# Kernel optimization log

Hardware: AMD Instinct MI355X
Metric: run time of the kernel (lower is better)

Reference implementation:

```python
import jax, jax.numpy as jnp
import numpy as np

N_NODES = 50000
N_EDGES = 800000
F_IN = 256
F_OUT = 64
HEADS = 4
LEAKY_ALPHA = 0.2


def setup_inputs() -> dict:
    key = jax.random.key(0)
    ks = jax.random.split(key, 8)
    x = jax.random.normal(ks[0], (N_NODES, F_IN), dtype=jnp.float32)
    W = jax.random.normal(ks[1], (HEADS, F_IN, F_OUT), dtype=jnp.float32) * 0.05
    a_self = jax.random.normal(ks[2], (HEADS, F_OUT), dtype=jnp.float32) * 0.05
    a_neigh = jax.random.normal(ks[3], (HEADS, F_OUT), dtype=jnp.float32) * 0.05
    bias = jnp.zeros((HEADS, F_OUT), dtype=jnp.float32)
    adj_val = jnp.ones((N_EDGES,), dtype=jnp.float32)
    edge_row = jax.random.randint(ks[4], (N_EDGES,), 0, N_NODES, dtype=jnp.int32)
    edge_col = jax.random.randint(ks[5], (N_EDGES,), 0, N_NODES, dtype=jnp.int32)
    return {"x": x, "W": W, "a_self": a_self, "a_neigh": a_neigh,
            "bias": bias, "adj_val": adj_val,
            "edge_row": edge_row, "edge_col": edge_col}


def reference(x, W, a_self, a_neigh, bias, adj_val, edge_row, edge_col):
    N = x.shape[0]
    # per-head projected features: [H, N, F_out]
    feats = jnp.einsum('nf,hfo->hno', x, W)
    # attention logits per node: [H, N]
    s_self = jnp.einsum('hno,ho->hn', feats, a_self)
    s_neigh = jnp.einsum('hno,ho->hn', feats, a_neigh)
    # edge scores at sparse adjacency positions: [H, E]
    z = s_self[:, edge_row] + s_neigh[:, edge_col]
    e = jnp.where(z > 0, z, LEAKY_ALPHA * z) * adj_val[None, :]

    def seg_softmax(e_h):
        # sparse softmax over each row's nonzero entries
        m = jax.ops.segment_max(e_h, edge_row, num_segments=N)
        ex = jnp.exp(e_h - m[edge_row])
        s = jax.ops.segment_sum(ex, edge_row, num_segments=N)
        return ex / s[edge_row]

    alpha = jax.vmap(seg_softmax)(e)  # [H, E]

    def aggregate(alpha_h, feat_h):
        # sparse-dense matmul: out[i] = sum_{j in N(i)} alpha_ij * feat[j]
        return jax.ops.segment_sum(alpha_h[:, None] * feat_h[edge_col],
                                   edge_row, num_segments=N)

    out = jax.vmap(aggregate)(alpha, feats) + bias[:, None, :]  # [H, N, F_out]
    # concat heads -> [N, H*F_out], then activation
    out = jnp.transpose(out, (1, 0, 2)).reshape(N, -1)
    return jax.nn.relu(out)
```

## Files before the change

### kernel.cpp

```cpp
#include <hip/hip_runtime.h>
#include <hip/hip_fp16.h>
#include <math.h>

#define NN 50000
#define NE 800000
#define FIN 256
#define FOUT 64
#define HEADS 4
#define HF 256
#define CAP 64
#define NBUCK 391
#define BROWS 128
#define CAPB 4096
#define BT_BLOCKS 32

typedef unsigned short u16;
typedef unsigned int u32;
typedef unsigned long long u64;
typedef __attribute__((ext_vector_type(4))) u16 u16x4;
typedef __attribute__((ext_vector_type(8))) u16 u16x8;
typedef __attribute__((ext_vector_type(8))) short short8;
typedef __attribute__((ext_vector_type(4))) float f32x4;

__device__ __forceinline__ u16 f2bf(float x) {
  u32 u = __float_as_uint(x);
  u += 0x7fffu + ((u >> 16) & 1u);
  return (u16)(u >> 16);
}
__device__ __forceinline__ float bf2f(u16 u) {
  return __uint_as_float(((u32)u) << 16);
}
__device__ __forceinline__ void gload_lds16(u16* lds, const u16* g) {
  __builtin_amdgcn_global_load_lds(
      (const __attribute__((address_space(1))) u32*)g,
      (__attribute__((address_space(3))) u32*)lds, 16, 0, 0);
}

__global__ __launch_bounds__(512) void binA_bt_k(const int* __restrict__ erow,
                                                 const int* __restrict__ ecol,
                                                 const float* __restrict__ adj,
                                                 int* __restrict__ cntA,
                                                 u64* __restrict__ coarse,
                                                 const float* __restrict__ W,
                                                 u16* __restrict__ Bt) {
  __shared__ int hist[NBUCK];
  __shared__ int gbase[NBUCK];
  const int tid = threadIdx.x;

  if (blockIdx.x >= NBUCK) {
    int t0 = (blockIdx.x - NBUCK) * 2048 + tid * 4;
    int ho = t0 >> 8, f0 = t0 & 255;
    int h = ho >> 6, o = ho & 63;
    const float* wp = W + h * (FIN * FOUT) + o;
    u16x4 v = { f2bf(wp[(f0 + 0) * FOUT]), f2bf(wp[(f0 + 1) * FOUT]),
                f2bf(wp[(f0 + 2) * FOUT]), f2bf(wp[(f0 + 3) * FOUT]) };
    *(u16x4*)&Bt[t0] = v;
    return;
  }

  for (int i = tid; i < NBUCK; i += 512) hist[i] = 0;
  __syncthreads();
  const int e0 = blockIdx.x * 2048 + tid;
  int bk[4], lr[4], rl[4], ok[4];
  u32 rec[4];
#pragma unroll
  for (int j = 0; j < 4; ++j) {
    int e = e0 + j * 512;
    ok[j] = (e < NE);
    int ee = ok[j] ? e : 0;
    int r = erow[ee];
    int c = ecol[ee];
    float av = adj[ee];
    __half ha = __float2half_rn(av);
    bk[j] = r >> 7;
    rl[j] = r & 127;
    rec[j] = (u32)c | ((u32)(*(u16*)&ha) << 16);
    lr[j] = ok[j] ? atomicAdd(&hist[bk[j]], 1) : 0;
  }
  __syncthreads();
  for (int i = tid; i < NBUCK; i += 512) {
    int h = hist[i];
    gbase[i] = h ? atomicAdd(&cntA[i * 16], h) : 0;
  }
  __syncthreads();
#pragma unroll
  for (int j = 0; j < 4; ++j) {
    if (ok[j]) {
      int pos = gbase[bk[j]] + lr[j];
      if (pos < CAPB) {
        u64 v = ((u64)rl[j] << 32) | (u64)rec[j];
        coarse[(size_t)bk[j] * CAPB + pos] = v;
      }
    }
  }
}

__global__ __launch_bounds__(512) void gemm_binB_k(const float* __restrict__ X,
                                                   const u16* __restrict__ Bt,
                                                   u16* __restrict__ C,
                                                   const float* __restrict__ a_self,
                                                   const float* __restrict__ a_neigh,
                                                   float* __restrict__ sself,
                                                   float* __restrict__ sneigh,
                                                   const int* __restrict__ cntA,
                                                   const u64* __restrict__ coarse,
                                                   int* __restrict__ cnt,
                                                   u32* __restrict__ slots,
                                                   int M) {
  __shared__ __align__(16) u16 smA[128 * 64];
  __shared__ __align__(16) u16 smB[256 * 64];
  __shared__ int lcnt[BROWS];
  const int tid = threadIdx.x;

  if (blockIdx.x >= NBUCK) {
    const int b = blockIdx.x - NBUCK;
    for (int i = tid; i < BROWS; i += 512) lcnt[i] = 0;
    __syncthreads();
    const int n = min(cntA[b * 16], CAPB);
    const u64* src = coarse + (size_t)b * CAPB;
    for (int i = tid; i < n; i += 512) {
      u64 v = src[i];
      int rl = (int)(v >> 32);
      u32 rec = (u32)v;
      int p = atomicAdd(&lcnt[rl], 1);
      if (p < CAP) slots[((size_t)(b * BROWS + rl)) * CAP + p] = rec;
    }
    __syncthreads();
    for (int i = tid; i < BROWS; i += 512) {
      int row = b * BROWS + i;
      if (row < NN) cnt[row] = min(lcnt[i], CAP);
    }
    return;
  }

  const int m0 = blockIdx.x * 128;
  const int lane = tid & 63, wid = tid >> 6;
  const int wr = wid >> 2, wc = wid & 3;
  const int arow = tid >> 3;
  const int acol = (tid & 7) * 8;
  f32x4 acc[4][4] = {};

  for (int k0 = 0; k0 < FIN; k0 += 64) {
    float4 p[2][2];
#pragma unroll
    for (int c = 0; c < 2; ++c) {
      int row = m0 + c * 64 + arow;
      if (row > M - 1) row = M - 1;
      const float* ap = X + (size_t)row * 256 + k0 + acol;
      p[c][0] = *(const float4*)ap;
      p[c][1] = *(const float4*)(ap + 4);
    }
#pragma unroll
    for (int c = 0; c < 4; ++c) {
      int row = c * 64 + arow;
      gload_lds16(&smB[(c * 64 + arow) * 64 + acol], Bt + row * 256 + k0 + acol);
    }
#pragma unroll
    for (int c = 0; c < 2; ++c) {
      u16x8 av = { f2bf(p[c][0].x), f2bf(p[c][0].y), f2bf(p[c][0].z), f2bf(p[c][0].w),
                   f2bf(p[c][1].x), f2bf(p[c][1].y), f2bf(p[c][1].z), f2bf(p[c][1].w) };
      *(u16x8*)&smA[(c * 64 + arow) * 64 + acol] = av;
    }
    asm volatile("s_waitcnt vmcnt(0)" ::: "memory");
    __syncthreads();
#pragma unroll
    for (int kk = 0; kk < 2; ++kk) {
      const int kb = kk * 32 + (lane >> 4) * 8;
      short8 aF[4], bF[4];
#pragma unroll
      for (int mi = 0; mi < 4; ++mi)
        aF[mi] = *(const short8*)&smA[(wr * 64 + mi * 16 + (lane & 15)) * 64 + kb];
#pragma unroll
      for (int ni = 0; ni < 4; ++ni)
        bF[ni] = *(const short8*)&smB[(wc * 64 + ni * 16 + (lane & 15)) * 64 + kb];
#pragma unroll
      for (int mi = 0; mi < 4; ++mi)
#pragma unroll
        for (int ni = 0; ni < 4; ++ni)
          acc[mi][ni] = __builtin_amdgcn_mfma_f32_16x16x32_bf16(aF[mi], bF[ni], acc[mi][ni], 0, 0, 0);
    }
    __syncthreads();
  }
#pragma unroll
  for (int mi = 0; mi < 4; ++mi) {
#pragma unroll
    for (int ni = 0; ni < 4; ++ni) {
      f32x4 a = acc[mi][ni];
      int col = wc * 64 + ni * 16 + (lane & 15);
#pragma unroll
      for (int r = 0; r < 4; ++r) {
        int row = m0 + wr * 64 + mi * 16 + (lane >> 4) * 4 + r;
        if (row < M) C[(size_t)row * 256 + col] = f2bf(a[r]);
      }
    }
  }
  float asv[4], anv[4];
#pragma unroll
  for (int ni = 0; ni < 4; ++ni) {
    int col = wc * 64 + ni * 16 + (lane & 15);
    asv[ni] = a_self[col];
    anv[ni] = a_neigh[col];
  }
#pragma unroll
  for (int mi = 0; mi < 4; ++mi) {
#pragma unroll
    for (int r = 0; r < 4; ++r) {
      float ds = 0.f, dn = 0.f;
#pragma unroll
      for (int ni = 0; ni < 4; ++ni) {
        float v = acc[mi][ni][r];
        ds = fmaf(v, asv[ni], ds);
        dn = fmaf(v, anv[ni], dn);
      }
#pragma unroll
      for (int off = 1; off < 16; off <<= 1) {
        ds += __shfl_xor(ds, off, 64);
        dn += __shfl_xor(dn, off, 64);
      }
      if ((lane & 15) == 0) {
        int row = m0 + wr * 64 + mi * 16 + (lane >> 4) * 4 + r;
        if (row < M) {
          sself[row * 4 + wc] = ds;
          sneigh[row * 4 + wc] = dn;
        }
      }
    }
  }
}

#define NODE_B 3125
__global__ __launch_bounds__(256) void node8_k(const int* __restrict__ cnt,
                                               const u32* __restrict__ slots,
                                               const float4* __restrict__ sself4,
                                               const float4* __restrict__ sneigh4,
                                               const u16* __restrict__ fb,
                                               const float* __restrict__ bias,
                                               float* __restrict__ out) {
  const int tid = threadIdx.x;
  const int l = tid & 31;
  const int hsel = l >> 4;
  const int hw0 = blockIdx.x * 8 + (tid >> 5);
  const float4 b0 = ((const float4*)bias)[l];
  const float4 b1 = ((const float4*)bias)[32 + l];

#pragma unroll
  for (int pass = 0; pass < 2; ++pass) {
    const int i = hw0 + pass * 25000;
    const int deg = cnt[i];
    const int beg = i * CAP;
    const float4 ssv = sself4[i];
    float s0 = 0.f, s1 = 0.f;
    float4 acc0 = { 0.f, 0.f, 0.f, 0.f };
    float4 acc1 = { 0.f, 0.f, 0.f, 0.f };

    for (int base = 0; base < deg; base += 32) {
      const int c32 = min(32, deg - base);
      u32 sv = slots[beg + base + min(l, c32 - 1)];
      int colv = (int)(sv & 0xFFFFu);

      int colq[8];
      u16x4 f0[8], f1[8];
#pragma unroll
      for (int q = 0; q < 8; ++q) colq[q] = __shfl(colv, q, 32);
#pragma unroll
      for (int q = 0; q < 8; ++q) {
        const u16* fp = fb + (size_t)colq[q] * HF + l * 4;
        f0[q] = *(const u16x4*)fp;
        f1[q] = *(const u16x4*)(fp + 128);
      }

      u16 ah = (u16)(sv >> 16);
      float av = __half2float(*(const __half*)&ah);
      float4 nb = sneigh4[colv];
      float z0 = ssv.x + nb.x, z1 = ssv.y + nb.y;
      float z2 = ssv.z + nb.z, z3 = ssv.w + nb.w;
      float w0 = __expf((z0 > 0.f ? z0 : 0.2f * z0) * av);
      float w1 = __expf((z1 > 0.f ? z1 : 0.2f * z1) * av);
      float w2 = __expf((z2 > 0.f ? z2 : 0.2f * z2) * av);
      float w3 = __expf((z3 > 0.f ? z3 : 0.2f * z3) * av);
      if (l >= c32) { w0 = 0.f; w1 = 0.f; w2 = 0.f; w3 = 0.f; }
      __half2 h01 = __floats2half2_rn(w0, w1);
      __half2 h23 = __floats2half2_rn(w2, w3);
      u32 wy = *(u32*)&h01, wz = *(u32*)&h23;

      const int c8 = (c32 + 7) & ~7;
      for (int e = 0; e < c8; e += 8) {
        float wa[8], wb[8];
#pragma unroll
        for (int q = 0; q < 8; ++q) {
          u32 y = (u32)__shfl((int)wy, e + q, 32);
          u32 z = (u32)__shfl((int)wz, e + q, 32);
          float2 fy = __half22float2(*(const __half2*)&y);
          float2 fz = __half22float2(*(const __half2*)&z);
          wa[q] = hsel ? fy.y : fy.x;
          wb[q] = hsel ? fz.y : fz.x;
        }
#pragma unroll
        for (int q = 0; q < 8; ++q) {
          s0 += wa[q];
          s1 += wb[q];
          acc0.x = fmaf(wa[q], bf2f(f0[q][0]), acc0.x);
          acc0.y = fmaf(wa[q], bf2f(f0[q][1]), acc0.y);
          acc0.z = fmaf(wa[q], bf2f(f0[q][2]), acc0.z);
          acc0.w = fmaf(wa[q], bf2f(f0[q][3]), acc0.w);
          acc1.x = fmaf(wb[q], bf2f(f1[q][0]), acc1.x);
          acc1.y = fmaf(wb[q], bf2f(f1[q][1]), acc1.y);
          acc1.z = fmaf(wb[q], bf2f(f1[q][2]), acc1.z);
          acc1.w = fmaf(wb[q], bf2f(f1[q][3]), acc1.w);
        }
        if (e + 8 < c8) {
#pragma unroll
          for (int q = 0; q < 8; ++q) colq[q] = __shfl(colv, e + 8 + q, 32);
#pragma unroll
          for (int q = 0; q < 8; ++q) {
            const u16* fp = fb + (size_t)colq[q] * HF + l * 4;
            f0[q] = *(const u16x4*)fp;
            f1[q] = *(const u16x4*)(fp + 128);
          }
        }
      }
    }
    const float rs0 = (s0 > 0.f) ? __frcp_rn(s0) : 0.f;
    const float rs1 = (s1 > 0.f) ? __frcp_rn(s1) : 0.f;
    float4 o0, o1;
    o0.x = fmaxf(fmaf(acc0.x, rs0, b0.x), 0.f);
    o0.y = fmaxf(fmaf(acc0.y, rs0, b0.y), 0.f);
    o0.z = fmaxf(fmaf(acc0.z, rs0, b0.z), 0.f);
    o0.w = fmaxf(fmaf(acc0.w, rs0, b0.w), 0.f);
    o1.x = fmaxf(fmaf(acc1.x, rs1, b1.x), 0.f);
    o1.y = fmaxf(fmaf(acc1.y, rs1, b1.y), 0.f);
    o1.z = fmaxf(fmaf(acc1.z, rs1, b1.z), 0.f);
    o1.w = fmaxf(fmaf(acc1.w, rs1, b1.w), 0.f);
    ((float4*)out)[(size_t)i * 64 + l] = o0;
    ((float4*)out)[(size_t)i * 64 + 32 + l] = o1;
  }
}

extern "C" void kernel_launch(void* const* d_in, const int* in_sizes, int n_in,
                              void* d_out, int out_size, void* d_ws, size_t ws_size,
                              hipStream_t stream) {
  const float* x       = (const float*)d_in[0];
  const float* W       = (const float*)d_in[1];
  const float* a_self  = (const float*)d_in[2];
  const float* a_neigh = (const float*)d_in[3];
  const float* bias    = (const float*)d_in[4];
  const float* adj     = (const float*)d_in[5];
  const int*   erow    = (const int*)d_in[6];
  const int*   ecol    = (const int*)d_in[7];
  float* out = (float*)d_out;

  char* w = (char*)d_ws;
  u16*   Bt     = (u16*)w;   w += 131072;
  u16*   fb     = (u16*)w;   w += 25600000;
  float* sself  = (float*)w; w += 800000;
  float* sneigh = (float*)w; w += 800000;
  int*   cntA   = (int*)w;   w += NBUCK * 16 * 4;
  int*   cnt    = (int*)w;   w += 200192;
  u32*   slots  = (u32*)w;   w += NN * CAP * 4;
  u64*   coarse = (u64*)w;   w += (size_t)NBUCK * CAPB * 8;

  hipMemsetAsync(cntA, 0, NBUCK * 16 * sizeof(int), stream);
  binA_bt_k<<<dim3(NBUCK + BT_BLOCKS), dim3(512), 0, stream>>>(erow, ecol, adj,
                                                               cntA, coarse, W, Bt);
  gemm_binB_k<<<dim3(NBUCK + NBUCK), dim3(512), 0, stream>>>(
      x, Bt, fb, a_self, a_neigh, sself, sneigh, cntA, coarse, cnt, slots, NN);
  node8_k<<<dim3(NODE_B), dim3(256), 0, stream>>>(cnt, slots,
                                                  (const float4*)sself,
                                                  (const float4*)sneigh,
                                                  fb, bias, out);
}
```

Baseline: 114.4 us.

## Fuse fine edge binning into node aggregation kernel via shared-memory slots

Moves the second-stage binning (coarse bucket to per-row slot lists) out of the GEMM kernel and into the aggregation kernel. Each block handles half a bucket, scatters that bucket's edges into per-row slot lists held in LDS, then aggregates those rows directly. This removes the global slots/cnt arrays and the round trip through them. The cost is that each coarse bucket is read twice, once per half-block, and the aggregation blocks are larger with more LDS use, which may lower occupancy.

```diff
diff --git a/kernel.cpp b/kernel.cpp
--- a/kernel.cpp
+++ b/kernel.cpp
@@ -11,6 +11,7 @@
 #define CAP 64
 #define NBUCK 391
 #define BROWS 128
+#define SROWS 64
 #define CAPB 4096
 #define BT_BLOCKS 32
 
@@ -95,44 +96,17 @@
   }
 }
 
-__global__ __launch_bounds__(512) void gemm_binB_k(const float* __restrict__ X,
-                                                   const u16* __restrict__ Bt,
-                                                   u16* __restrict__ C,
-                                                   const float* __restrict__ a_self,
-                                                   const float* __restrict__ a_neigh,
-                                                   float* __restrict__ sself,
-                                                   float* __restrict__ sneigh,
-                                                   const int* __restrict__ cntA,
-                                                   const u64* __restrict__ coarse,
-                                                   int* __restrict__ cnt,
-                                                   u32* __restrict__ slots,
-                                                   int M) {
+__global__ __launch_bounds__(512) void gemm_lg_k(const float* __restrict__ X,
+                                                 const u16* __restrict__ Bt,
+                                                 u16* __restrict__ C,
+                                                 const float* __restrict__ a_self,
+                                                 const float* __restrict__ a_neigh,
+                                                 float* __restrict__ sself,
+                                                 float* __restrict__ sneigh,
+                                                 int M) {
   __shared__ __align__(16) u16 smA[128 * 64];
   __shared__ __align__(16) u16 smB[256 * 64];
-  __shared__ int lcnt[BROWS];
   const int tid = threadIdx.x;
-
-  if (blockIdx.x >= NBUCK) {
-    const int b = blockIdx.x - NBUCK;
-    for (int i = tid; i < BROWS; i += 512) lcnt[i] = 0;
-    __syncthreads();
-    const int n = min(cntA[b * 16], CAPB);
-    const u64* src = coarse + (size_t)b * CAPB;
-    for (int i = tid; i < n; i += 512) {
-      u64 v = src[i];
-      int rl = (int)(v >> 32);
-      u32 rec = (u32)v;
-      int p = atomicAdd(&lcnt[rl], 1);
-      if (p < CAP) slots[((size_t)(b * BROWS + rl)) * CAP + p] = rec;
-    }
-    __syncthreads();
-    for (int i = tid; i < BROWS; i += 512) {
-      int row = b * BROWS + i;
-      if (row < NN) cnt[row] = min(lcnt[i], CAP);
-    }
-    return;
-  }
-
   const int m0 = blockIdx.x * 128;
   const int lane = tid & 63, wid = tid >> 6;
   const int wr = wid >> 2, wc = wid & 3;
@@ -228,34 +202,53 @@
   }
 }
 
-#define NODE_B 3125
-__global__ __launch_bounds__(256) void node8_k(const int* __restrict__ cnt,
-                                               const u32* __restrict__ slots,
-                                               const float4* __restrict__ sself4,
-                                               const float4* __restrict__ sneigh4,
-                                               const u16* __restrict__ fb,
-                                               const float* __restrict__ bias,
-                                               float* __restrict__ out) {
+__global__ __launch_bounds__(512) void binB_node_k(const int* __restrict__ cntA,
+                                                   const u64* __restrict__ coarse,
+                                                   const float4* __restrict__ sself4,
+                                                   const float4* __restrict__ sneigh4,
+                                                   const u16* __restrict__ fb,
+                                                   const float* __restrict__ bias,
+                                                   float* __restrict__ out) {
+  __shared__ u32 slds[SROWS * CAP];
+  __shared__ int lcnt[SROWS];
   const int tid = threadIdx.x;
+  const int b = blockIdx.x >> 1;
+  const int half = blockIdx.x & 1;
+  const int lo = half * SROWS;
+
+  for (int i = tid; i < SROWS; i += 512) lcnt[i] = 0;
+  __syncthreads();
+  const int n = min(cntA[b * 16], CAPB);
+  const u64* src = coarse + (size_t)b * CAPB;
+  for (int i = tid; i < n; i += 512) {
+    u64 v = src[i];
+    int rl = (int)(v >> 32) - lo;
+    if ((unsigned)rl < SROWS) {
+      int p = atomicAdd(&lcnt[rl], 1);
+      if (p < CAP) slds[rl * CAP + p] = (u32)v;
+    }
+  }
+  __syncthreads();
+
   const int l = tid & 31;
   const int hsel = l >> 4;
-  const int hw0 = blockIdx.x * 8 + (tid >> 5);
+  const int hw = tid >> 5;
   const float4 b0 = ((const float4*)bias)[l];
   const float4 b1 = ((const float4*)bias)[32 + l];
 
-#pragma unroll
-  for (int pass = 0; pass < 2; ++pass) {
-    const int i = hw0 + pass * 25000;
-    const int deg = cnt[i];
-    const int beg = i * CAP;
-    const float4 ssv = sself4[i];
+  for (int rl = hw; rl < SROWS; rl += 16) {
+    const int row = b * BROWS + lo + rl;
+    if (row >= NN) continue;
+    const int deg = min(lcnt[rl], CAP);
+    const u32* sl = &slds[rl * CAP];
+    const float4 ssv = sself4[row];
     float s0 = 0.f, s1 = 0.f;
     float4 acc0 = { 0.f, 0.f, 0.f, 0.f };
     float4 acc1 = { 0.f, 0.f, 0.f, 0.f };
 
     for (int base = 0; base < deg; base += 32) {
       const int c32 = min(32, deg - base);
-      u32 sv = slots[beg + base + min(l, c32 - 1)];
+      u32 sv = sl[base + min(l, c32 - 1)];
       int colv = (int)(sv & 0xFFFFu);
 
       int colq[8];
@@ -331,8 +324,8 @@
     o1.y = fmaxf(fmaf(acc1.y, rs1, b1.y), 0.f);
     o1.z = fmaxf(fmaf(acc1.z, rs1, b1.z), 0.f);
     o1.w = fmaxf(fmaf(acc1.w, rs1, b1.w), 0.f);
-    ((float4*)out)[(size_t)i * 64 + l] = o0;
-    ((float4*)out)[(size_t)i * 64 + 32 + l] = o1;
+    ((float4*)out)[(size_t)row * 64 + l] = o0;
+    ((float4*)out)[(size_t)row * 64 + 32 + l] = o1;
   }
 }
 
@@ -355,17 +348,15 @@
   float* sself  = (float*)w; w += 800000;
   float* sneigh = (float*)w; w += 800000;
   int*   cntA   = (int*)w;   w += NBUCK * 16 * 4;
-  int*   cnt    = (int*)w;   w += 200192;
-  u32*   slots  = (u32*)w;   w += NN * CAP * 4;
   u64*   coarse = (u64*)w;   w += (size_t)NBUCK * CAPB * 8;
 
   hipMemsetAsync(cntA, 0, NBUCK * 16 * sizeof(int), stream);
   binA_bt_k<<<dim3(NBUCK + BT_BLOCKS), dim3(512), 0, stream>>>(erow, ecol, adj,
                                                                cntA, coarse, W, Bt);
-  gemm_binB_k<<<dim3(NBUCK + NBUCK), dim3(512), 0, stream>>>(
-      x, Bt, fb, a_self, a_neigh, sself, sneigh, cntA, coarse, cnt, slots, NN);
-  node8_k<<<dim3(NODE_B), dim3(256), 0, stream>>>(cnt, slots,
-                                                  (const float4*)sself,
-                                                  (const float4*)sneigh,
-                                                  fb, bias, out);
-}
+  gemm_lg_k<<<dim3((NN + 127) / 128), dim3(512), 0, stream>>>(x, Bt, fb, a_self, a_neigh,
+                                                              sself, sneigh, NN);
+  binB_node_k<<<dim3(NBUCK * 2), dim3(512), 0, stream>>>(cntA, coarse,
+                                                         (const float4*)sself,
+                                                         (const float4*)sneigh,
+                                                         fb, bias, out);
+}
```

After: 131.0 us. 1.15x slower.
